# Optimization experiments

Measured on AMD Instinct MI355X. Metric: run time of the kernel, lower is better.

## Reference

```python
import jax, jax.numpy as jnp
import numpy as np

L = 1024   # latent_size
K = 8
R = L // K # 128 reduced dim
T = 32     # caption length
B = 64     # batch (images and captions)
DIN = 300  # word embedding dim
REG = 36   # image regions
R3 = 3 * R
H3 = 3 * L

def _p(key, shape, scale=0.05):
    return scale * jax.random.normal(key, shape, dtype=jnp.float32)

def setup_inputs():
    ks = jax.random.split(jax.random.key(0), 40)
    return {
        'img_embed': jax.random.normal(ks[0], (B, REG, L), jnp.float32),
        'cap_embed': jax.random.normal(ks[1], (B, T, DIN), jnp.float32),
        'lens': jax.random.randint(ks[2], (B,), 1, T + 1),
        'W_reduce_img': _p(ks[3], (R, L)), 'b_reduce_img': _p(ks[4], (R,)),
        'W_reduce_txt': _p(ks[5], (R, DIN)), 'b_reduce_txt': _p(ks[6], (R,)),
        'gru_Wih_f': _p(ks[7], (H3, DIN)), 'gru_Whh_f': _p(ks[8], (H3, L)),
        'gru_bih_f': _p(ks[9], (H3,)), 'gru_bhh_f': _p(ks[10], (H3,)),
        'gru_Wih_b': _p(ks[11], (H3, DIN)), 'gru_Whh_b': _p(ks[12], (H3, L)),
        'gru_bih_b': _p(ks[13], (H3,)), 'gru_bhh_b': _p(ks[14], (H3,)),
        'sa_Wq': _p(ks[15], (R, L)), 'sa_bq': _p(ks[16], (R,)),
        'sa_Wk': _p(ks[17], (R, L)), 'sa_bk': _p(ks[18], (R,)),
        'sa_Wv': _p(ks[19], (L, L)), 'sa_bv': _p(ks[20], (L,)),
        'sa_gamma': jnp.float32(0.5),
        'gen_Wih': _p(ks[21], (R3 * R, R)), 'gen_bih': _p(ks[22], (R3 * R,)),
        'gen_Whh': _p(ks[23], (R3 * R, R)), 'gen_bhh': _p(ks[24], (R3 * R,)),
        'gen_Wbih': _p(ks[25], (R3, R)), 'gen_bbih': _p(ks[26], (R3,)),
        'gen_Wbhh': _p(ks[27], (R3, R)), 'gen_bbhh': _p(ks[28], (R3,)),
        'W_txt_fc': _p(ks[29], (L, R + L)), 'b_txt_fc': _p(ks[30], (L,)),
    }

def l2norm(x, axis=-1, eps=1e-8):
    return x / (jnp.linalg.norm(x, axis=axis, keepdims=True) + eps)

def gru_dir(x, Wih, Whh, bih, bhh, reverse=False):
    # torch GRU math, gate order [r, z, n]; x: (B, T, D) -> (B, T, H)
    H = Whh.shape[1]
    gi = jnp.einsum('btd,hd->tbh', x, Wih) + bih  # precompute input gates (T, B, 3H)
    h0 = jnp.zeros((x.shape[0], H), x.dtype)
    def step(h, gi_t):
        gh = h @ Whh.T + bhh
        r = jax.nn.sigmoid(gi_t[:, :H] + gh[:, :H])
        z = jax.nn.sigmoid(gi_t[:, H:2 * H] + gh[:, H:2 * H])
        n = jnp.tanh(gi_t[:, 2 * H:] + r * gh[:, 2 * H:])
        hn = (1.0 - z) * n + z * h
        return hn, hn
    _, hs = jax.lax.scan(step, h0, gi, reverse=reverse)
    return jnp.swapaxes(hs, 0, 1)

def _forward(img_embed, cap_embed, lens, W_reduce_img, b_reduce_img, W_reduce_txt, b_reduce_txt,
             gru_Wih_f, gru_Whh_f, gru_bih_f, gru_bhh_f, gru_Wih_b, gru_Whh_b, gru_bih_b, gru_bhh_b,
             sa_Wq, sa_bq, sa_Wk, sa_bk, sa_Wv, sa_bv, sa_gamma,
             gen_Wih, gen_bih, gen_Whh, gen_bhh, gen_Wbih, gen_bbih, gen_Wbhh, gen_bbhh,
             W_txt_fc, b_txt_fc):
    # 1. bidirectional GRU over captions, average the two directions
    hf = gru_dir(cap_embed, gru_Wih_f, gru_Whh_f, gru_bih_f, gru_bhh_f, False)
    hb = gru_dir(cap_embed, gru_Wih_b, gru_Whh_b, gru_bih_b, gru_bhh_b, True)
    txt = (hf + hb) / 2.0                                   # (B, T, L)
    # 2. SAGAN-style 1D self-attention on (B, L, T)
    x = jnp.swapaxes(txt, 1, 2)                             # (B, L, T)
    q = jnp.einsum('bct,oc->bto', x, sa_Wq) + sa_bq          # (B, T, R)
    kk = jnp.einsum('bct,oc->bot', x, sa_Wk) + sa_bk[:, None]  # (B, R, T)
    attn = jax.nn.softmax(jnp.einsum('bto,bos->bts', q, kk), axis=-1)  # (B, T, T)
    v = jnp.einsum('bct,oc->bot', x, sa_Wv) + sa_bv[:, None]  # (B, L, T)
    x = sa_gamma * jnp.einsum('bcs,bts->bct', v, attn) + x
    # 3. length-masked mean pooling
    txt = jnp.swapaxes(x, 1, 2)                             # (B, T, L)
    mask = (jnp.arange(T)[None, :] < lens[:, None]).astype(txt.dtype)
    txt_embed = (txt * mask[:, :, None]).sum(1) / lens[:, None].astype(txt.dtype)  # (B, L)
    # 4. conv1d(k=1) reductions == linear over channel dim
    img = jnp.swapaxes(img_embed, 1, 2)                     # (B, L, REG)
    img_embed_global = img.mean(-1)                         # (B, L)
    cap_reduced = jnp.einsum('btd,od->btd2'.replace('d2','o'), cap_embed, W_reduce_txt) + b_reduce_txt  # (B, T, R)
    img_reduced = jnp.einsum('bcr,oc->bor', img, W_reduce_img) + b_reduce_img[:, None]  # (B, R, REG)
    img_global_vec = img_reduced.mean(-1)                   # (B, R)
    # 5. per-image generated-weight GRU over all captions (vmap replaces B-loop)
    def per_image(base, img_glob):
        Wih = (gen_Wih @ base + gen_bih).reshape(R3, R)
        Whh = (gen_Whh @ base + gen_bhh).reshape(R3, R)
        bih = gen_Wbih @ base + gen_bbih
        bhh = gen_Wbhh @ base + gen_bbhh
        gi = jnp.einsum('btd,hd->tbh', cap_reduced, Wih) + bih  # (T, B, 3R)
        h0 = jnp.zeros((cap_reduced.shape[0], R), cap_reduced.dtype)
        def step(h, gi_t):
            gh = h @ Whh.T + bhh
            r = jax.nn.sigmoid(gi_t[:, :R] + gh[:, :R])
            z = jax.nn.sigmoid(gi_t[:, R:2 * R] + gh[:, R:2 * R])
            n = jnp.tanh(gi_t[:, 2 * R:] + r * gh[:, 2 * R:])
            hn = (1.0 - z) * n + z * h
            return hn, hn
        _, hs = jax.lax.scan(step, h0, gi)                  # (T, B, R)
        txt_vec = hs.max(0)                                 # max over time -> (B, R)
        txt_vec = jnp.concatenate([txt_embed, txt_vec], axis=1) @ W_txt_fc.T + b_txt_fc
        txt_vec = l2norm(txt_vec)                           # (B, L)
        iv = l2norm(img_glob)                               # (L,)
        return txt_vec @ iv                                 # (B,) cosine sims for this image
    sims = jax.vmap(per_image)(img_global_vec, img_embed_global)  # (B_img, B_cap)
    return sims

def reference(img_embed, cap_embed, lens, W_reduce_img, b_reduce_img, W_reduce_txt, b_reduce_txt,
              gru_Wih_f, gru_Whh_f, gru_bih_f, gru_bhh_f, gru_Wih_b, gru_Whh_b, gru_bih_b, gru_bhh_b,
              sa_Wq, sa_bq, sa_Wk, sa_bk, sa_Wv, sa_bv, sa_gamma,
              gen_Wih, gen_bih, gen_Whh, gen_bhh, gen_Wbih, gen_bbih, gen_Wbhh, gen_bbhh,
              W_txt_fc, b_txt_fc):
    return _forward(img_embed, cap_embed, lens, W_reduce_img, b_reduce_img, W_reduce_txt, b_reduce_txt,
                    gru_Wih_f, gru_Whh_f, gru_bih_f, gru_bhh_f, gru_Wih_b, gru_Whh_b, gru_bih_b, gru_bhh_b,
                    sa_Wq, sa_bq, sa_Wk, sa_bk, sa_Wv, sa_bv, sa_gamma,
                    gen_Wih, gen_bih, gen_Whh, gen_bhh, gen_Wbih, gen_bbih, gen_Wbhh, gen_bbhh,
                    W_txt_fc, b_txt_fc)
```

## Files before the change

### kernel.cpp

```cpp
#include <hip/hip_runtime.h>
#include <math.h>

#define Lsz   1024
#define Tsz   32
#define Bsz   64
#define DIN   300
#define REG   36
#define Rsz   128
#define R3sz  384
#define H3sz  3072
#define GENROWS 49152
#define NC    2048
#define KPAD  304

typedef __attribute__((ext_vector_type(8))) short bf16x8;
typedef __attribute__((ext_vector_type(4))) float f32x4;

__device__ __forceinline__ float sigf(float x) { return 1.f / (1.f + __expf(-x)); }

__device__ __forceinline__ ushort f2bf(float x) {
    unsigned u = __float_as_uint(x);
    unsigned r = (u + 0x7fffu + ((u >> 16) & 1u)) >> 16;
    return (ushort)r;
}
__device__ __forceinline__ float bf2f(ushort h) {
    return __uint_as_float((unsigned)h << 16);
}


__device__ __forceinline__ size_t hfrag_off(int k, int b) {
    return (((size_t)(k >> 5) * 4 + (b >> 4)) * 64 +
            ((((k >> 3) & 3) << 4) | (b & 15))) * 8 + (k & 7);
}

__device__ __forceinline__ void pack8(const float* v, ushort* dsth, ushort* dstl) {
    unsigned hw[4], lw[4];
#pragma unroll
    for (int e2 = 0; e2 < 4; e2++) {
        ushort h0 = f2bf(v[2 * e2]);
        ushort h1 = f2bf(v[2 * e2 + 1]);
        ushort l0 = f2bf(v[2 * e2] - bf2f(h0));
        ushort l1 = f2bf(v[2 * e2 + 1] - bf2f(h1));
        hw[e2] = (unsigned)h0 | ((unsigned)h1 << 16);
        lw[e2] = (unsigned)l0 | ((unsigned)l1 << 16);
    }
    *(uint4*)dsth = make_uint4(hw[0], hw[1], hw[2], hw[3]);
    *(uint4*)dstl = make_uint4(lw[0], lw[1], lw[2], lw[3]);
}

__global__ __launch_bounds__(256) void transp_kernel(
    const float* __restrict__ in, float* __restrict__ out,
    int R, int Cin, int Cpad, int lda, int woff)
{
    __shared__ float s[64][65];
    int c0 = blockIdx.x * 64, r0 = blockIdx.y * 64;
    int tid = threadIdx.x;
#pragma unroll
    for (int l = 0; l < 16; l++) {
        int e = l * 256 + tid;
        int rr = e >> 6, cc = e & 63;
        int r = r0 + rr, c = c0 + cc;
        s[rr][cc] = (r < R && c < Cin) ? in[(size_t)r * lda + woff + c] : 0.f;
    }
    __syncthreads();
#pragma unroll
    for (int l = 0; l < 16; l++) {
        int e = l * 256 + tid;
        int cc = e >> 6, rr = e & 63;
        int c = c0 + cc, r = r0 + rr;
        if (c < Cpad && r < R) out[(size_t)c * R + r] = s[rr][cc];
    }
}

__global__ __launch_bounds__(256) void captr_kernel(
    const float* __restrict__ cap_embed, float* __restrict__ capTr)
{
    __shared__ float s[64][65];
    int t = blockIdx.x, kc = blockIdx.y;
    int tid = threadIdx.x;
#pragma unroll
    for (int l = 0; l < 16; l++) {
        int e = l * 256 + tid;
        int b = e >> 6, kk = e & 63;
        int k = kc * 64 + kk;
// ... 298 lines not shown
    for (int c = tid; c < Lsz; c += 256) {
        float s = 0.f;
        for (int r = 0; r < REG; r++) s += img_embed[((size_t)i * REG + r) * Lsz + c];
        row[c] = s * (1.f / (float)REG);
    }
    __syncthreads();
    float ss = 0.f;
    for (int c = tid; c < Lsz; c += 256) { float x = row[c]; ss = fmaf(x, x, ss); }
#pragma unroll
    for (int off = 32; off; off >>= 1) ss += __shfl_down(ss, off, 64);
    int lane = tid & 63, w = tid >> 6;
    if (lane == 0) ps[w] = ss;
    __syncthreads();
    float inv = 1.f / (sqrtf(ps[0] + ps[1] + ps[2] + ps[3]) + 1e-8f);
    for (int c = tid; c < Lsz; c += 256)
        iv[(size_t)i * Lsz + c] = row[c] * inv;
    for (int o = w * 32; o < w * 32 + 32; o++) {
        float a = 0.f;
        const float* wr = W_reduce_img + (size_t)o * Lsz + lane * 16;
        const float* rr = row + lane * 16;
#pragma unroll
        for (int u = 0; u < 16; u++) a = fmaf(wr[u], rr[u], a);
#pragma unroll
        for (int off = 32; off; off >>= 1) a += __shfl_down(a, off, 64);
        if (lane == 0) base[(size_t)i * Rsz + o] = a + b_reduce_img[o];
    }
}

__global__ __launch_bounds__(256) void packwhh_kernel(
    const float* __restrict__ Wf, const float* __restrict__ Wb,
    float* __restrict__ WFh_, float* __restrict__ WFl_)
{
    int tid = threadIdx.x;
    int l = tid & 63, wid = tid >> 6;
    int k0 = blockIdx.x * 4 + wid;
    int mstrip = blockIdx.y;
    int dir = blockIdx.z;
    const float* W = dir ? Wb : Wf;
    int row = mstrip * 16 + (l & 15);
    int col = k0 * 32 + (l >> 4) * 8;
    float v[8];
    *(float4*)&v[0] = *(const float4*)&W[(size_t)row * Lsz + col];
    *(float4*)&v[4] = *(const float4*)&W[(size_t)row * Lsz + col + 4];
    size_t off = ((size_t)(dir * 192 + mstrip) * 32 + k0) * 512 + l * 8;
    pack8(v, (ushort*)WFh_ + off, (ushort*)WFl_ + off);
}

__global__ __launch_bounds__(256) void packgenw_kernel(
    const float* __restrict__ WihAllT, const float* __restrict__ WhhAllT,
    float* __restrict__ GFh_, float* __restrict__ GFl_)
{
    int tid = threadIdx.x;
    int l = tid & 63, kt = tid >> 6;
    int mstrip = blockIdx.x;
    int mat = blockIdx.y;
    int i = blockIdx.z;
    const float* W = (mat ? WhhAllT : WihAllT) + (size_t)i * GENROWS;
    int row = mstrip * 16 + (l & 15);
    int kb = kt * 32 + (l >> 4) * 8;
    float v[8];
#pragma unroll
    for (int e = 0; e < 8; e++)
        v[e] = W[(size_t)(kb + e) * R3sz + row];
    size_t off = (((size_t)(i * 2 + mat) * 24 + mstrip) * 4 + kt) * 512 + l * 8;
    pack8(v, (ushort*)GFh_ + off, (ushort*)GFl_ + off);
}

__global__ __launch_bounds__(256) void packcap_kernel(
    const float* __restrict__ capT2, float* __restrict__ CFh_, float* __restrict__ CFl_)
{
    int tid = threadIdx.x;
    int l = tid & 63, kt = tid >> 6;
    int ctp = blockIdx.x;
    int col = ctp * 16 + (l & 15);
    int kb = kt * 32 + (l >> 4) * 8;
    float v[8];
#pragma unroll
    for (int e = 0; e < 8; e++)
        v[e] = capT2[(size_t)(kb + e) * NC + col];
    size_t off = ((size_t)kt * 128 + ctp) * 512 + l * 8;
    pack8(v, (ushort*)CFh_ + off, (ushort*)CFl_ + off);
}

__global__ __launch_bounds__(256) void step_fused(
    const float* __restrict__ WhhF_h, const float* __restrict__ WhhF_l,
    const float* __restrict__ WgenF_h, const float* __restrict__ WgenF_l,
    const float* __restrict__ capF_h, const float* __restrict__ capF_l,
    float* __restrict__ capHF_h, float* __restrict__ capHF_l,
    float* __restrict__ genHF_h, float* __restrict__ genHF_l,
    const float* __restrict__ giT2_f, const float* __restrict__ giT2_b,
    float* __restrict__ hfT, float* __restrict__ hbT,
    const float* __restrict__ bhh_f, const float* __restrict__ bhh_b,
    const float* __restrict__ bihAll, const float* __restrict__ bhhAll,
    const float* __restrict__ hprevT, float* __restrict__ hcurT,
    float* __restrict__ hmaxT, int step)
{
    __shared__ float red[48 * 256];
    int tid = threadIdx.x, l = tid & 63, wid = tid >> 6;
    int bid = blockIdx.x;
    int ping = (step & 1) ^ 1;
    int pong = step & 1;

    if (bid < 128) {
        int dir = bid >> 6, js = bid & 63;
        f32x4 acc[3][4];
#pragma unroll
        for (int g = 0; g < 3; g++)
#pragma unroll
            for (int ct = 0; ct < 4; ct++) acc[g][ct] = (f32x4){0.f, 0.f, 0.f, 0.f};

        if (step > 0) {
            const ushort* Wh = (const ushort*)WhhF_h + (size_t)dir * (192 * 32 * 512);
            const ushort* Wl = (const ushort*)WhhF_l + (size_t)dir * (192 * 32 * 512);
            const ushort* Hh = (const ushort*)capHF_h + (size_t)(dir * 2 + ping) * 65536;
            const ushort* Hl = (const ushort*)capHF_l + (size_t)(dir * 2 + ping) * 65536;
            for (int k8 = 0; k8 < 8; k8++) {
                int k0 = wid * 8 + k8;
                bf16x8 Bh[4], Bl[4], Ah[3], Al[3];
#pragma unroll
                for (int ct = 0; ct < 4; ct++) {
                    size_t fo = ((size_t)k0 * 4 + ct) * 512 + l * 8;
                    Bh[ct] = *(const bf16x8*)(Hh + fo);
                    Bl[ct] = *(const bf16x8*)(Hl + fo);
                }
#pragma unroll
                for (int g = 0; g < 3; g++) {
                    size_t fo = ((size_t)(g * 64 + js) * 32 + k0) * 512 + l * 8;
                    Ah[g] = *(const bf16x8*)(Wh + fo);
                    Al[g] = *(const bf16x8*)(Wl + fo);
                }
#pragma unroll
                for (int g = 0; g < 3; g++)
#pragma unroll
                    for (int ct = 0; ct < 4; ct++)
                        acc[g][ct] = __builtin_amdgcn_mfma_f32_16x16x32_bf16(
                            Ah[g], Bh[ct], acc[g][ct], 0, 0, 0);
#pragma unroll
                for (int g = 0; g < 3; g++)
#pragma unroll
                    for (int ct = 0; ct < 4; ct++)
                        acc[g][ct] = __builtin_amdgcn_mfma_f32_16x16x32_bf16(
                            Ah[g], Bl[ct], acc[g][ct], 0, 0, 0);
#pragma unroll
                for (int g = 0; g < 3; g++)
#pragma unroll
                    for (int ct = 0; ct < 4; ct++)
                        acc[g][ct] = __builtin_amdgcn_mfma_f32_16x16x32_bf16(
                            Al[g], Bh[ct], acc[g][ct], 0, 0, 0);
            }
        }
#pragma unroll
        for (int g = 0; g < 3; g++)
#pragma unroll
            for (int ct = 0; ct < 4; ct++)
                *(f32x4*)&red[((wid * 3 + g) * 4 + ct) * 256 + l * 4] = acc[g][ct];
        __syncthreads();

        const float* giT = dir ? giT2_b : giT2_f;
        float* hT        = dir ? hbT   : hfT;
        const float* bhh = dir ? bhh_b : bhh_f;
        int t  = dir ? (Tsz - 1 - step) : step;
        int tp = dir ? (t + 1) : (t - 1);
        ushort* Ch = (ushort*)capHF_h + (size_t)(dir * 2 + pong) * 65536;
        ushort* Cl = (ushort*)capHF_l + (size_t)(dir * 2 + pong) * 65536;
#pragma unroll
        for (int u = 0; u < 4; u++) {
            int e = u * 256 + tid;
            int jj = e >> 6, b = e & 63;
            int j = js * 16 + jj;
            float gh[3] = {0.f, 0.f, 0.f};
            if (step > 0) {
                int lane_ = ((jj >> 2) << 4) | (b & 15);
                int reg = jj & 3, ct = b >> 4;
#pragma unroll
                for (int w = 0; w < 4; w++)
#pragma unroll
                    for (int g = 0; g < 3; g++)
                        gh[g] += red[((w * 3 + g) * 4 + ct) * 256 + lane_ * 4 + reg];
            }
            size_t gc = (size_t)t * 64 + b;
            float gr = giT[(size_t)j * NC + gc];
            float gz = giT[((size_t)Lsz + j) * NC + gc];
            float gn = giT[((size_t)2 * Lsz + j) * NC + gc];
            float hp = (step > 0) ? hT[((size_t)tp * Lsz + j) * Bsz + b] : 0.f;
            float r = sigf(gr + gh[0] + bhh[j]);
            float z = sigf(gz + gh[1] + bhh[Lsz + j]);
            float n = tanhf(gn + r * (gh[2] + bhh[2 * Lsz + j]));
            float h = (1.f - z) * n + z * hp;
            hT[((size_t)t * Lsz + j) * Bsz + b] = h;
            size_t fo = hfrag_off(j, b);
            ushort hb = f2bf(h);
            Ch[fo] = hb;
            Cl[fo] = f2bf(h - bf2f(hb));
        }
    } else {
        int g2 = bid - 128;
        int i = g2 >> 2;
        int p = g2 & 3;
        int mat = wid & 1;
        int sl = wid >> 1;
        int strip = p * 2 + sl;
        f32x4 acc[3][4];
#pragma unroll
        for (int g = 0; g < 3; g++)
#pragma unroll
            for (int ct = 0; ct < 4; ct++) acc[g][ct] = (f32x4){0.f, 0.f, 0.f, 0.f};

        if (mat == 0 || step > 0) {
            const ushort* Ahp = (const ushort*)WgenF_h + (size_t)(i * 2 + mat) * 96 * 512;
            const ushort* Alp = (const ushort*)WgenF_l + (size_t)(i * 2 + mat) * 96 * 512;
            const ushort* Bhp;
            const ushort* Blp;
            if (mat == 0) {
                Bhp = (const ushort*)capF_h;
                Blp = (const ushort*)capF_l;
            } else {
                Bhp = (const ushort*)genHF_h + (size_t)(ping * 64 + i) * 8192;
                Blp = (const ushort*)genHF_l + (size_t)(ping * 64 + i) * 8192;
            }
            for (int kt = 0; kt < 4; kt++) {
                bf16x8 Bh[4], Bl[4], Ah[3], Al[3];
#pragma unroll
                for (int ct = 0; ct < 4; ct++) {
                    size_t fo = (mat == 0)
                        ? ((size_t)kt * 128 + step * 4 + ct) * 512 + l * 8
                        : ((size_t)kt * 4 + ct) * 512 + l * 8;
                    Bh[ct] = *(const bf16x8*)(Bhp + fo);
                    Bl[ct] = *(const bf16x8*)(Blp + fo);
                }
#pragma unroll
                for (int g = 0; g < 3; g++) {
                    size_t fo = ((size_t)(g * 8 + strip) * 4 + kt) * 512 + l * 8;
                    Ah[g] = *(const bf16x8*)(Ahp + fo);
                    Al[g] = *(const bf16x8*)(Alp + fo);
                }
#pragma unroll
                for (int g = 0; g < 3; g++)
#pragma unroll
                    for (int ct = 0; ct < 4; ct++)
                        acc[g][ct] = __builtin_amdgcn_mfma_f32_16x16x32_bf16(
                            Ah[g], Bh[ct], acc[g][ct], 0, 0, 0);
#pragma unroll
                for (int g = 0; g < 3; g++)
#pragma unroll
                    for (int ct = 0; ct < 4; ct++)
                        acc[g][ct] = __builtin_amdgcn_mfma_f32_16x16x32_bf16(
                            Ah[g], Bl[ct], acc[g][ct], 0, 0, 0);
#pragma unroll
                for (int g = 0; g < 3; g++)
#pragma unroll
                    for (int ct = 0; ct < 4; ct++)
                        acc[g][ct] = __builtin_amdgcn_mfma_f32_16x16x32_bf16(
                            Al[g], Bh[ct], acc[g][ct], 0, 0, 0);
            }
        }
#pragma unroll
        for (int g = 0; g < 3; g++)
#pragma unroll
            for (int ct = 0; ct < 4; ct++)
                *(f32x4*)&red[(((sl * 2 + mat) * 3 + g) * 4 + ct) * 256 + l * 4] = acc[g][ct];
        __syncthreads();

        const float* bih = bihAll + (size_t)i * R3sz;
        const float* bhh = bhhAll + (size_t)i * R3sz;
        ushort* Gh = (ushort*)genHF_h + (size_t)(pong * 64 + i) * 8192;
        ushort* Gl = (ushort*)genHF_l + (size_t)(pong * 64 + i) * 8192;
#pragma unroll
        for (int u = 0; u < 8; u++) {
            int e = u * 256 + tid;
            int sl2 = e >> 10;
            int jj = (e >> 6) & 15;
            int b = e & 63;
            int j = (p * 2 + sl2) * 16 + jj;
            int lane_ = ((jj >> 2) << 4) | (b & 15);
            int reg = jj & 3, ct = b >> 4;
            float sih[3], shh[3];
#pragma unroll
            for (int g = 0; g < 3; g++) {
                sih[g] = red[(((sl2 * 2 + 0) * 3 + g) * 4 + ct) * 256 + lane_ * 4 + reg];
                shh[g] = (step > 0)
                    ? red[(((sl2 * 2 + 1) * 3 + g) * 4 + ct) * 256 + lane_ * 4 + reg]
                    : 0.f;
            }
            float r = sigf(sih[0] + bih[j] + shh[0] + bhh[j]);
            float z = sigf(sih[1] + bih[Rsz + j] + shh[1] + bhh[Rsz + j]);
            float n = tanhf(sih[2] + bih[2 * Rsz + j] + r * (shh[2] + bhh[2 * Rsz + j]));
            float hp = (step > 0) ? hprevT[((size_t)i * Rsz + j) * Bsz + b] : 0.f;
            float h = (1.f - z) * n + z * hp;
            size_t idx = ((size_t)i * Rsz + j) * Bsz + b;
            hcurT[idx] = h;
            hmaxT[idx] = (step == 0) ? h : fmaxf(hmaxT[idx], h);
            size_t fo = hfrag_off(j, b);
            ushort hb = f2bf(h);
            Gh[fo] = hb;
            Gl[fo] = f2bf(h - bf2f(hb));
        }
    }
}

__global__ __launch_bounds__(256) void txt_combine(
    const float* __restrict__ hfT, const float* __restrict__ hbT,
    float* __restrict__ txt, float* __restrict__ txtT)
{
    __shared__ float s[64][65];
    int t = blockIdx.x;
    int c0 = blockIdx.y * 64;
    int tid = threadIdx.x;
#pragma unroll
    for (int l = 0; l < 16; l++) {
        int e = l * 256 + tid;
        int cc = e >> 6, b = e & 63;
        size_t idx = ((size_t)t * Lsz + c0 + cc) * Bsz + b;
        s[cc][b] = 0.5f * (hfT[idx] + hbT[idx]);
    }
    __syncthreads();
#pragma unroll
    for (int l = 0; l < 16; l++) {
        int e = l * 256 + tid;
        int b = e >> 6, cc = e & 63;
        txt[((size_t)b * Tsz + t) * Lsz + c0 + cc] = s[cc][b];
    }
#pragma unroll
    for (int l = 0; l < 16; l++) {
        int e = l * 256 + tid;
        int cc = e >> 6, b = e & 63;
        txtT[(size_t)(c0 + cc) * NC + t * 64 + b] = s[cc][b];
    }
}

__global__ __launch_bounds__(256) void attn_kernel(
    const float* __restrict__ q, const float* __restrict__ kmat,
    const float* __restrict__ vP, const float* __restrict__ sa_bv,
    const float* __restrict__ txt,
    const float* __restrict__ gamma_p, float* __restrict__ xattn)
{
    __shared__ float qs[32][129];
    __shared__ float ks[32][129];
    __shared__ float Sc[32][33];
    __shared__ float vs[128][33];
    int b = blockIdx.x;
    int c0 = blockIdx.y * 128;
    int tid = threadIdx.x;
    for (int e = tid; e < Tsz * Rsz; e += 256) {
        qs[e >> 7][e & 127] = q[(size_t)b * Tsz * Rsz + e];
        ks[e >> 7][e & 127] = kmat[(size_t)b * Tsz * Rsz + e];
    }
    for (int e = tid; e < 128 * 32; e += 256) {
        int cc = e >> 5, ss = e & 31;
        size_t base = (size_t)(c0 + cc) * NC + ss * 64 + b;
        float v = sa_bv[c0 + cc];
#pragma unroll
        for (int z = 0; z < 2; z++)
            v += vP[(size_t)z * Lsz * NC + base];
        vs[cc][ss] = v;
    }
    __syncthreads();
    for (int e = tid; e < Tsz * Tsz; e += 256) {
        int t = e >> 5, ss = e & 31;
        float acc = 0.f;
#pragma unroll 4
        for (int o = 0; o < Rsz; o++) acc = fmaf(qs[t][o], ks[ss][o], acc);
        Sc[t][ss] = acc;
    }
    __syncthreads();
    if (tid < 32) {
        int t = tid;
        float mx = -1e30f;
#pragma unroll
        for (int ss = 0; ss < 32; ss++) mx = fmaxf(mx, Sc[t][ss]);
        float sum = 0.f;
        float ex[32];
#pragma unroll
        for (int ss = 0; ss < 32; ss++) { ex[ss] = __expf(Sc[t][ss] - mx); sum += ex[ss]; }
        float inv = 1.f / sum;
#pragma unroll
        for (int ss = 0; ss < 32; ss++) Sc[t][ss] = ex[ss] * inv;
    }
    __syncthreads();
// ... 70 lines not shown
        int c = cs * 256 + w * 64 + u;
        float f = fcT[(size_t)c * 4096 + i * 64 + b] + base_fcT[(size_t)c * Bsz + b] + bfc[c];
        s1 = fmaf(f, f, s1);
        s2 = fmaf(f, iv[(size_t)i * Lsz + c], s2);
    }
    int m = i * 64 + b;
    atomicAdd(&accA[m], s1);
    atomicAdd(&accB[m], s2);
}

__global__ __launch_bounds__(256) void sims_final(
    const float* __restrict__ accA, const float* __restrict__ accB,
    float* __restrict__ out)
{
    int m = blockIdx.x * 256 + threadIdx.x;
    out[m] = accB[m] / (sqrtf(accA[m]) + 1e-8f);
}

extern "C" void kernel_launch(void* const* d_in, const int* in_sizes, int n_in,
                              void* d_out, int out_size, void* d_ws, size_t ws_size,
                              hipStream_t stream)
{
    const float* img_embed    = (const float*)d_in[0];
    const float* cap_embed    = (const float*)d_in[1];
    const int*   lens         = (const int*)d_in[2];
    const float* W_reduce_img = (const float*)d_in[3];
    const float* b_reduce_img = (const float*)d_in[4];
    const float* W_reduce_txt = (const float*)d_in[5];
    const float* b_reduce_txt = (const float*)d_in[6];
    const float* gru_Wih_f    = (const float*)d_in[7];
    const float* gru_Whh_f    = (const float*)d_in[8];
    const float* gru_bih_f    = (const float*)d_in[9];
    const float* gru_bhh_f    = (const float*)d_in[10];
    const float* gru_Wih_b    = (const float*)d_in[11];
    const float* gru_Whh_b    = (const float*)d_in[12];
    const float* gru_bih_b    = (const float*)d_in[13];
    const float* gru_bhh_b    = (const float*)d_in[14];
    const float* sa_Wq        = (const float*)d_in[15];
    const float* sa_bq        = (const float*)d_in[16];
    const float* sa_Wk        = (const float*)d_in[17];
    const float* sa_bk        = (const float*)d_in[18];
    const float* sa_Wv        = (const float*)d_in[19];
    const float* sa_bv        = (const float*)d_in[20];
    const float* sa_gamma     = (const float*)d_in[21];
    const float* gen_Wih      = (const float*)d_in[22];
    const float* gen_bih      = (const float*)d_in[23];
    const float* gen_Whh      = (const float*)d_in[24];
    const float* gen_bhh      = (const float*)d_in[25];
    const float* gen_Wbih     = (const float*)d_in[26];
    const float* gen_bbih     = (const float*)d_in[27];
    const float* gen_Wbhh     = (const float*)d_in[28];
    const float* gen_bbhh     = (const float*)d_in[29];
    const float* W_txt_fc     = (const float*)d_in[30];
    const float* b_txt_fc     = (const float*)d_in[31];

    float* ws = (float*)d_ws;
    size_t off = 0;
    auto alloc = [&](size_t n) { float* p = ws + off; off += n; return p; };
    float* giT2_f   = alloc((size_t)H3sz * NC);
    float* giT2_b   = alloc((size_t)H3sz * NC);
    float* hfT      = alloc((size_t)Tsz * Lsz * Bsz);
    float* hbT      = alloc((size_t)Tsz * Lsz * Bsz);
    float* capTr    = alloc((size_t)KPAD * NC);
    float* capT2    = alloc((size_t)Rsz * NC);
    float* txt      = alloc((size_t)Bsz * Tsz * Lsz);
    float* txtT     = alloc((size_t)Lsz * NC);
    float* qbuf     = alloc((size_t)Bsz * Tsz * Rsz);
    float* kbuf     = alloc((size_t)Bsz * Tsz * Rsz);
    float* pool     = alloc((size_t)12582912);
    float* WhhFh  = pool;
    float* WhhFl  = pool + 3145728;
    float* WgenFh = pool + 6291456;
    float* WgenFl = pool + 9437184;
    float* qP  = pool;
    float* kP  = pool + 2097152;
    float* vP  = pool + 4194304;
    float* fcT = pool + 8388608;
    float* xattn    = alloc((size_t)Bsz * Tsz * Lsz);
    float* txt_emb  = alloc((size_t)Bsz * Lsz);
    float* base     = alloc((size_t)Bsz * Rsz);
    float* iv       = alloc((size_t)Bsz * Lsz);
    float* WihAllT  = alloc((size_t)Bsz * GENROWS);
    float* WhhAllT  = alloc((size_t)Bsz * GENROWS);
    float* WihT_f   = alloc((size_t)KPAD * H3sz);
    float* WihT_b   = alloc((size_t)KPAD * H3sz);
    float* WrtT     = alloc((size_t)KPAD * Rsz);
    float* WvT      = alloc((size_t)Lsz * Lsz);
    float* WqT      = alloc((size_t)Lsz * Rsz);
    float* WkT      = alloc((size_t)Lsz * Rsz);
    float* WfcT     = alloc((size_t)Rsz * Lsz);
    float* bihAll   = alloc((size_t)Bsz * R3sz);
    float* bhhAll   = alloc((size_t)Bsz * R3sz);
    float* hA       = alloc((size_t)Bsz * Rsz * Bsz);
    float* hB       = alloc((size_t)Bsz * Rsz * Bsz);
    float* hmaxT    = alloc((size_t)Bsz * Rsz * Bsz);
    float* hstdT    = alloc((size_t)Rsz * Bsz * Bsz);
    float* base_fcT = alloc((size_t)Lsz * Bsz);
    float* accA     = alloc(4096);
    float* accB     = alloc(4096);
    float* capFh    = alloc(131072);
    float* capFl    = alloc(131072);
    float* capHFh   = alloc(131072);
    float* capHFl   = alloc(131072);
    float* genHFh   = alloc(524288);
    float* genHFl   = alloc(524288);

    hipMemsetAsync(accA, 0, 2 * 4096 * sizeof(float), stream);

    transp_kernel<<<dim3(5, 48), 256, 0, stream>>>(gru_Wih_f, WihT_f, H3sz, DIN, KPAD, DIN, 0);
    transp_kernel<<<dim3(5, 48), 256, 0, stream>>>(gru_Wih_b, WihT_b, H3sz, DIN, KPAD, DIN, 0);
    transp_kernel<<<dim3(5, 2), 256, 0, stream>>>(W_reduce_txt, WrtT, Rsz, DIN, KPAD, DIN, 0);
    transp_kernel<<<dim3(16, 16), 256, 0, stream>>>(sa_Wv, WvT, Lsz, Lsz, Lsz, Lsz, 0);
    transp_kernel<<<dim3(16, 2), 256, 0, stream>>>(sa_Wq, WqT, Rsz, Lsz, Lsz, Lsz, 0);
    transp_kernel<<<dim3(16, 2), 256, 0, stream>>>(sa_Wk, WkT, Rsz, Lsz, Lsz, Lsz, 0);
    transp_kernel<<<dim3(2, 16), 256, 0, stream>>>(W_txt_fc, WfcT, Lsz, Rsz, Rsz, Rsz + Lsz, Lsz);
    captr_kernel<<<dim3(32, 5), 256, 0, stream>>>(cap_embed, capTr);

    img_kernel<<<64, 256, 0, stream>>>(img_embed, W_reduce_img, b_reduce_img, base, iv);
    genw_gemm<<<dim3(3, 129, 2), 256, 0, stream>>>(gen_Wih, gen_bih, gen_Whh, gen_bhh,
        gen_Wbih, gen_bbih, gen_Wbhh, gen_bbhh, base, WihAllT, WhhAllT, bihAll, bhhAll);
    packwhh_kernel<<<dim3(8, 192, 2), 256, 0, stream>>>(gru_Whh_f, gru_Whh_b, WhhFh, WhhFl);
    packgenw_kernel<<<dim3(24, 2, 64), 256, 0, stream>>>(WihAllT, WhhAllT, WgenFh, WgenFl);

    gemm_tt<<<dim3(16, 24, 2), 256, 0, stream>>>(WihT_f, WihT_b, capTr,
        gru_bih_f, gru_bih_b, giT2_f, giT2_b, H3sz);
    gemm_tt<<<dim3(16, 1, 1), 256, 0, stream>>>(WrtT, WrtT, capTr,
        b_reduce_txt, b_reduce_txt, capT2, capT2, Rsz);
    packcap_kernel<<<128, 256, 0, stream>>>(capT2, capFh, capFl);

    for (int s = 0; s < Tsz; s++) {
        const float* hp = (s & 1) ? hA : hB;
        float* hc = (s & 1) ? hB : hA;
        if (s == 0) hp = hA;
        step_fused<<<384, 256, 0, stream>>>(WhhFh, WhhFl, WgenFh, WgenFl,
            capFh, capFl, capHFh, capHFl, genHFh, genHFl,
            giT2_f, giT2_b, hfT, hbT, gru_bhh_f, gru_bhh_b,
            bihAll, bhhAll, hp, hc, hmaxT, s);
    }
    hstdT_kernel<<<64, 256, 0, stream>>>(hmaxT, hstdT);

    txt_combine<<<dim3(32, 16), 256, 0, stream>>>(hfT, hbT, txt, txtT);
    gemm_qk<<<dim3(16, 2, 8), 256, 0, stream>>>(WqT, WkT, txtT, qP, kP);
    gemm_ttp<<<dim3(16, 8, 2), 256, 0, stream>>>(WvT, txtT, vP, Lsz, NC, 512);
    qkc_kernel<<<dim3(32, 2), 256, 0, stream>>>(qP, kP, sa_bq, sa_bk, qbuf, kbuf);
    attn_kernel<<<dim3(64, 8), 256, 0, stream>>>(qbuf, kbuf, vP, sa_bv, txt,
        sa_gamma, xattn);

    pool_kernel<<<dim3(64, 4), 256, 0, stream>>>(xattn, lens, txt_emb);
    basefc_kernel<<<256, 256, 0, stream>>>(txt_emb, W_txt_fc, base_fcT);

    gemm_ttp<<<dim3(32, 8, 1), 256, 0, stream>>>(WfcT, hstdT, fcT, Lsz, 4096, Rsz);
    sims_part<<<dim3(64, 4), 256, 0, stream>>>(fcT, base_fcT, b_txt_fc, iv, accA, accB);
    sims_final<<<16, 256, 0, stream>>>(accA, accB, (float*)d_out);
}
```

Before: 1.363 ms.

## Make GRU recurrence one persistent cooperative kernel and move input-gate GEMM to MFMA

```diff
diff --git a/kernel.cpp b/kernel.cpp
--- a/kernel.cpp
+++ b/kernel.cpp
@@ -1,5 +1,8 @@
 #include <hip/hip_runtime.h>
+#include <hip/hip_cooperative_groups.h>
 #include <math.h>
+
+namespace cg = cooperative_groups;
 
 #define Lsz   1024
 #define Tsz   32
@@ -464,218 +467,337 @@
     pack8(v, (ushort*)CFh_ + off, (ushort*)CFl_ + off);
 }
 
-__global__ __launch_bounds__(256) void step_fused(
+__global__ __launch_bounds__(256) void packwih_kernel(
+    const float* __restrict__ Wf, const float* __restrict__ Wb,
+    float* __restrict__ Fh, float* __restrict__ Fl)
+{
+    int tid = threadIdx.x, l = tid & 63, wid = tid >> 6;
+    int kt = blockIdx.x * 4 + wid;
+    int m = blockIdx.y, dir = blockIdx.z;
+    if (kt >= 10) return;
+    const float* W = dir ? Wb : Wf;
+    int row = m * 16 + (l & 15);
+    int kb = kt * 32 + (l >> 4) * 8;
+    float v[8];
+#pragma unroll
+    for (int e = 0; e < 8; e++) {
+        int k = kb + e;
+        v[e] = (k < DIN) ? W[(size_t)row * DIN + k] : 0.f;
+    }
+    size_t off = (((size_t)dir * 192 + m) * 10 + kt) * 512 + l * 8;
+    pack8(v, (ushort*)Fh + off, (ushort*)Fl + off);
+}
+
+__global__ __launch_bounds__(256) void packcapb_kernel(
+    const float* __restrict__ cap_embed, float* __restrict__ Fh, float* __restrict__ Fl)
+{
+    int tid = threadIdx.x, l = tid & 63, wid = tid >> 6;
+    int ct = blockIdx.x;
+    int kt = blockIdx.y * 4 + wid;
+    if (kt >= 10) return;
+    int c = ct * 16 + (l & 15), t = c >> 6, b = c & 63;
+    int kb = kt * 32 + (l >> 4) * 8;
+    float v[8];
+#pragma unroll
+    for (int e = 0; e < 8; e++) {
+        int k = kb + e;
+        v[e] = (k < DIN) ? cap_embed[((size_t)b * Tsz + t) * DIN + k] : 0.f;
+    }
+    size_t off = ((size_t)kt * 128 + ct) * 512 + l * 8;
+    pack8(v, (ushort*)Fh + off, (ushort*)Fl + off);
+}
+
+__global__ __launch_bounds__(256) void gi_mfma(
+    const float* __restrict__ WihF_h, const float* __restrict__ WihF_l,
+    const float* __restrict__ capBF_h, const float* __restrict__ capBF_l,
+    const float* __restrict__ bih_f, const float* __restrict__ bih_b,
+    float* __restrict__ giT2_f, float* __restrict__ giT2_b)
+{
+    __shared__ __align__(16) ushort BsH[8][512];
+    __shared__ __align__(16) ushort BsL[8][512];
+    int tid = threadIdx.x, l = tid & 63, wid = tid >> 6;
+    int ctg = blockIdx.x, mg = blockIdx.y, dir = blockIdx.z;
+    int ct0 = ctg * 8;
+    int m0 = mg * 8 + wid * 2;
+    const ushort* AH = (const ushort*)WihF_h + (size_t)dir * (192 * 10 * 512);
+    const ushort* AL = (const ushort*)WihF_l + (size_t)dir * (192 * 10 * 512);
+    const ushort* BH = (const ushort*)capBF_h;
+    const ushort* BL = (const ushort*)capBF_l;
+    const float* bias = dir ? bih_b : bih_f;
+    float* C = dir ? giT2_b : giT2_f;
+
+    f32x4 acc[2][8];
+#pragma unroll
+    for (int m = 0; m < 2; m++)
+#pragma unroll
+        for (int ct = 0; ct < 8; ct++) acc[m][ct] = (f32x4){0.f, 0.f, 0.f, 0.f};
+
+    for (int kt = 0; kt < 10; kt++) {
+        __syncthreads();
+#pragma unroll
+        for (int u = 0; u < 2; u++) {
+            int e = u * 256 + tid;
+            int ct = e >> 6, p8 = (e & 63) * 8;
+            *(uint4*)&BsH[ct][p8] = *(const uint4*)&BH[((size_t)kt * 128 + ct0 + ct) * 512 + p8];
+            *(uint4*)&BsL[ct][p8] = *(const uint4*)&BL[((size_t)kt * 128 + ct0 + ct) * 512 + p8];
+        }
+        __syncthreads();
+        bf16x8 Ah[2], Al[2];
+#pragma unroll
+        for (int m = 0; m < 2; m++) {
+            size_t ao = ((size_t)(m0 + m) * 10 + kt) * 512 + l * 8;
+            Ah[m] = *(const bf16x8*)(AH + ao);
+            Al[m] = *(const bf16x8*)(AL + ao);
+        }
+#pragma unroll
+        for (int ct = 0; ct < 8; ct++) {
+            bf16x8 Bh = *(const bf16x8*)&BsH[ct][l * 8];
+            bf16x8 Bl = *(const bf16x8*)&BsL[ct][l * 8];
+#pragma unroll
+            for (int m = 0; m < 2; m++) {
+                acc[m][ct] = __builtin_amdgcn_mfma_f32_16x16x32_bf16(Ah[m], Bh, acc[m][ct], 0, 0, 0);
+                acc[m][ct] = __builtin_amdgcn_mfma_f32_16x16x32_bf16(Ah[m], Bl, acc[m][ct], 0, 0, 0);
+                acc[m][ct] = __builtin_amdgcn_mfma_f32_16x16x32_bf16(Al[m], Bh, acc[m][ct], 0, 0, 0);
+            }
+        }
+    }
+    int row4 = (l >> 4) * 4, col = l & 15;
+#pragma unroll
+    for (int m = 0; m < 2; m++) {
+        int nb_ = (m0 + m) * 16 + row4;
+#pragma unroll
+        for (int r = 0; r < 4; r++) {
+            float bv = bias[nb_ + r];
+#pragma unroll
+            for (int ct = 0; ct < 8; ct++)
+                C[(size_t)(nb_ + r) * NC + (size_t)(ct0 + ct) * 16 + col] = acc[m][ct][r] + bv;
+        }
+    }
+}
+
+template <bool COOP>
+__global__ __launch_bounds__(256) void rec_kernel(
     const float* __restrict__ WhhF_h, const float* __restrict__ WhhF_l,
     const float* __restrict__ WgenF_h, const float* __restrict__ WgenF_l,
     const float* __restrict__ capF_h, const float* __restrict__ capF_l,
-    float* __restrict__ capHF_h, float* __restrict__ capHF_l,
-    float* __restrict__ genHF_h, float* __restrict__ genHF_l,
+    float* capHF_h, float* capHF_l,
+    float* genHF_h, float* genHF_l,
     const float* __restrict__ giT2_f, const float* __restrict__ giT2_b,
-    float* __restrict__ hfT, float* __restrict__ hbT,
+    float* hfT, float* hbT,
     const float* __restrict__ bhh_f, const float* __restrict__ bhh_b,
     const float* __restrict__ bihAll, const float* __restrict__ bhhAll,
-    const float* __restrict__ hprevT, float* __restrict__ hcurT,
-    float* __restrict__ hmaxT, int step)
+    float* hA, float* hB, float* hmaxT,
+    int s0, int s1)
 {
     __shared__ float red[48 * 256];
     int tid = threadIdx.x, l = tid & 63, wid = tid >> 6;
     int bid = blockIdx.x;
-    int ping = (step & 1) ^ 1;
-    int pong = step & 1;
-
-    if (bid < 128) {
-        int dir = bid >> 6, js = bid & 63;
-        f32x4 acc[3][4];
-#pragma unroll
-        for (int g = 0; g < 3; g++)
-#pragma unroll
-            for (int ct = 0; ct < 4; ct++) acc[g][ct] = (f32x4){0.f, 0.f, 0.f, 0.f};
-
-        if (step > 0) {
-            const ushort* Wh = (const ushort*)WhhF_h + (size_t)dir * (192 * 32 * 512);
-            const ushort* Wl = (const ushort*)WhhF_l + (size_t)dir * (192 * 32 * 512);
-            const ushort* Hh = (const ushort*)capHF_h + (size_t)(dir * 2 + ping) * 65536;
-            const ushort* Hl = (const ushort*)capHF_l + (size_t)(dir * 2 + ping) * 65536;
-            for (int k8 = 0; k8 < 8; k8++) {
-                int k0 = wid * 8 + k8;
-                bf16x8 Bh[4], Bl[4], Ah[3], Al[3];
-#pragma unroll
-                for (int ct = 0; ct < 4; ct++) {
-                    size_t fo = ((size_t)k0 * 4 + ct) * 512 + l * 8;
-                    Bh[ct] = *(const bf16x8*)(Hh + fo);
-                    Bl[ct] = *(const bf16x8*)(Hl + fo);
+
+    for (int s = s0; s < s1; ++s) {
+        int ping = (s & 1) ^ 1;
+        int pong = s & 1;
+
+        if (bid < 128) {
+            int dir = bid >> 6, js = bid & 63;
+            f32x4 acc[3][4];
+#pragma unroll
+            for (int g = 0; g < 3; g++)
+#pragma unroll
+                for (int ct = 0; ct < 4; ct++) acc[g][ct] = (f32x4){0.f, 0.f, 0.f, 0.f};
+
+            if (s > 0) {
+                const ushort* Wh = (const ushort*)WhhF_h + (size_t)dir * (192 * 32 * 512);
+                const ushort* Wl = (const ushort*)WhhF_l + (size_t)dir * (192 * 32 * 512);
+                const ushort* Hh = (const ushort*)capHF_h + (size_t)(dir * 2 + ping) * 65536;
+                const ushort* Hl = (const ushort*)capHF_l + (size_t)(dir * 2 + ping) * 65536;
+                for (int k8 = 0; k8 < 8; k8++) {
+                    int k0 = wid * 8 + k8;
+                    bf16x8 Bh[4], Bl[4], Ah[3], Al[3];
+#pragma unroll
+                    for (int ct = 0; ct < 4; ct++) {
+                        size_t fo = ((size_t)k0 * 4 + ct) * 512 + l * 8;
+                        Bh[ct] = *(const bf16x8*)(Hh + fo);
+                        Bl[ct] = *(const bf16x8*)(Hl + fo);
+                    }
+#pragma unroll
+                    for (int g = 0; g < 3; g++) {
+                        size_t fo = ((size_t)(g * 64 + js) * 32 + k0) * 512 + l * 8;
+                        Ah[g] = *(const bf16x8*)(Wh + fo);
+                        Al[g] = *(const bf16x8*)(Wl + fo);
+                    }
+#pragma unroll
+                    for (int g = 0; g < 3; g++)
+#pragma unroll
+                        for (int ct = 0; ct < 4; ct++)
+                            acc[g][ct] = __builtin_amdgcn_mfma_f32_16x16x32_bf16(
+                                Ah[g], Bh[ct], acc[g][ct], 0, 0, 0);
+#pragma unroll
+                    for (int g = 0; g < 3; g++)
+#pragma unroll
+                        for (int ct = 0; ct < 4; ct++)
+                            acc[g][ct] = __builtin_amdgcn_mfma_f32_16x16x32_bf16(
+                                Ah[g], Bl[ct], acc[g][ct], 0, 0, 0);
+#pragma unroll
+                    for (int g = 0; g < 3; g++)
+#pragma unroll
+                        for (int ct = 0; ct < 4; ct++)
+                            acc[g][ct] = __builtin_amdgcn_mfma_f32_16x16x32_bf16(
+                                Al[g], Bh[ct], acc[g][ct], 0, 0, 0);
                 }
-#pragma unroll
-                for (int g = 0; g < 3; g++) {
-                    size_t fo = ((size_t)(g * 64 + js) * 32 + k0) * 512 + l * 8;
-                    Ah[g] = *(const bf16x8*)(Wh + fo);
-                    Al[g] = *(const bf16x8*)(Wl + fo);
+            }
+#pragma unroll
+            for (int g = 0; g < 3; g++)
+#pragma unroll
+                for (int ct = 0; ct < 4; ct++)
+                    *(f32x4*)&red[((wid * 3 + g) * 4 + ct) * 256 + l * 4] = acc[g][ct];
+            __syncthreads();
+
+            const float* giT = dir ? giT2_b : giT2_f;
+            float* hT        = dir ? hbT   : hfT;
+            const float* bhh = dir ? bhh_b : bhh_f;
+            int t  = dir ? (Tsz - 1 - s) : s;
+            int tp = dir ? (t + 1) : (t - 1);
+            ushort* Ch = (ushort*)capHF_h + (size_t)(dir * 2 + pong) * 65536;
+            ushort* Cl = (ushort*)capHF_l + (size_t)(dir * 2 + pong) * 65536;
+#pragma unroll
+            for (int u = 0; u < 4; u++) {
+                int e = u * 256 + tid;
+                int jj = e >> 6, b = e & 63;
+                int j = js * 16 + jj;
+                float gh[3] = {0.f, 0.f, 0.f};
+                if (s > 0) {
+                    int lane_ = ((jj >> 2) << 4) | (b & 15);
+                    int reg = jj & 3, ct = b >> 4;
+#pragma unroll
+                    for (int w = 0; w < 4; w++)
+#pragma unroll
+                        for (int g = 0; g < 3; g++)
+                            gh[g] += red[((w * 3 + g) * 4 + ct) * 256 + lane_ * 4 + reg];
                 }
-#pragma unroll
-                for (int g = 0; g < 3; g++)
-#pragma unroll
-                    for (int ct = 0; ct < 4; ct++)
-                        acc[g][ct] = __builtin_amdgcn_mfma_f32_16x16x32_bf16(
-                            Ah[g], Bh[ct], acc[g][ct], 0, 0, 0);
-#pragma unroll
-                for (int g = 0; g < 3; g++)
-#pragma unroll
-                    for (int ct = 0; ct < 4; ct++)
-                        acc[g][ct] = __builtin_amdgcn_mfma_f32_16x16x32_bf16(
-                            Ah[g], Bl[ct], acc[g][ct], 0, 0, 0);
-#pragma unroll
-                for (int g = 0; g < 3; g++)
-#pragma unroll
-                    for (int ct = 0; ct < 4; ct++)
-                        acc[g][ct] = __builtin_amdgcn_mfma_f32_16x16x32_bf16(
-                            Al[g], Bh[ct], acc[g][ct], 0, 0, 0);
+                size_t gc = (size_t)t * 64 + b;
+                float gr = giT[(size_t)j * NC + gc];
+                float gz = giT[((size_t)Lsz + j) * NC + gc];
+                float gn = giT[((size_t)2 * Lsz + j) * NC + gc];
+                float hp = (s > 0) ? hT[((size_t)tp * Lsz + j) * Bsz + b] : 0.f;
+                float r = sigf(gr + gh[0] + bhh[j]);
+                float z = sigf(gz + gh[1] + bhh[Lsz + j]);
+                float n = tanhf(gn + r * (gh[2] + bhh[2 * Lsz + j]));
+                float h = (1.f - z) * n + z * hp;
+                hT[((size_t)t * Lsz + j) * Bsz + b] = h;
+                size_t fo = hfrag_off(j, b);
+                ushort hb = f2bf(h);
+                Ch[fo] = hb;
+                Cl[fo] = f2bf(h - bf2f(hb));
             }
-        }
-#pragma unroll
-        for (int g = 0; g < 3; g++)
-#pragma unroll
-            for (int ct = 0; ct < 4; ct++)
-                *(f32x4*)&red[((wid * 3 + g) * 4 + ct) * 256 + l * 4] = acc[g][ct];
-        __syncthreads();
-
-        const float* giT = dir ? giT2_b : giT2_f;
-        float* hT        = dir ? hbT   : hfT;
-        const float* bhh = dir ? bhh_b : bhh_f;
-        int t  = dir ? (Tsz - 1 - step) : step;
-        int tp = dir ? (t + 1) : (t - 1);
-        ushort* Ch = (ushort*)capHF_h + (size_t)(dir * 2 + pong) * 65536;
-        ushort* Cl = (ushort*)capHF_l + (size_t)(dir * 2 + pong) * 65536;
-#pragma unroll
-        for (int u = 0; u < 4; u++) {
-            int e = u * 256 + tid;
-            int jj = e >> 6, b = e & 63;
-            int j = js * 16 + jj;
-            float gh[3] = {0.f, 0.f, 0.f};
-            if (step > 0) {
+        } else {
+            int g2 = bid - 128;
+            int i = g2 >> 2;
+            int p = g2 & 3;
+            int mat = wid & 1;
+            int sl = wid >> 1;
+            int strip = p * 2 + sl;
+            float* hcurT = (s & 1) ? hB : hA;
+            const float* hprevT = (s & 1) ? hA : hB;
+            f32x4 acc[3][4];
+#pragma unroll
+            for (int g = 0; g < 3; g++)
+#pragma unroll
+                for (int ct = 0; ct < 4; ct++) acc[g][ct] = (f32x4){0.f, 0.f, 0.f, 0.f};
+
+            if (mat == 0 || s > 0) {
+                const ushort* Ahp = (const ushort*)WgenF_h + (size_t)(i * 2 + mat) * 96 * 512;
+                const ushort* Alp = (const ushort*)WgenF_l + (size_t)(i * 2 + mat) * 96 * 512;
+                const ushort* Bhp;
+                const ushort* Blp;
+                if (mat == 0) {
+                    Bhp = (const ushort*)capF_h;
+                    Blp = (const ushort*)capF_l;
+                } else {
+                    Bhp = (const ushort*)genHF_h + (size_t)(ping * 64 + i) * 8192;
+                    Blp = (const ushort*)genHF_l + (size_t)(ping * 64 + i) * 8192;
+                }
+                for (int kt = 0; kt < 4; kt++) {
+                    bf16x8 Bh[4], Bl[4], Ah[3], Al[3];
+#pragma unroll
+                    for (int ct = 0; ct < 4; ct++) {
+                        size_t fo = (mat == 0)
+                            ? ((size_t)kt * 128 + s * 4 + ct) * 512 + l * 8
+                            : ((size_t)kt * 4 + ct) * 512 + l * 8;
+                        Bh[ct] = *(const bf16x8*)(Bhp + fo);
+                        Bl[ct] = *(const bf16x8*)(Blp + fo);
+                    }
+#pragma unroll
+                    for (int g = 0; g < 3; g++) {
+                        size_t fo = ((size_t)(g * 8 + strip) * 4 + kt) * 512 + l * 8;
+                        Ah[g] = *(const bf16x8*)(Ahp + fo);
+                        Al[g] = *(const bf16x8*)(Alp + fo);
+                    }
+#pragma unroll
+                    for (int g = 0; g < 3; g++)
+#pragma unroll
+                        for (int ct = 0; ct < 4; ct++)
+                            acc[g][ct] = __builtin_amdgcn_mfma_f32_16x16x32_bf16(
+                                Ah[g], Bh[ct], acc[g][ct], 0, 0, 0);
+#pragma unroll
+                    for (int g = 0; g < 3; g++)
+#pragma unroll
+                        for (int ct = 0; ct < 4; ct++)
+                            acc[g][ct] = __builtin_amdgcn_mfma_f32_16x16x32_bf16(
+                                Ah[g], Bl[ct], acc[g][ct], 0, 0, 0);
+#pragma unroll
+                    for (int g = 0; g < 3; g++)
+#pragma unroll
+                        for (int ct = 0; ct < 4; ct++)
+                            acc[g][ct] = __builtin_amdgcn_mfma_f32_16x16x32_bf16(
+                                Al[g], Bh[ct], acc[g][ct], 0, 0, 0);
+                }
+            }
+#pragma unroll
+            for (int g = 0; g < 3; g++)
+#pragma unroll
+                for (int ct = 0; ct < 4; ct++)
+                    *(f32x4*)&red[(((sl * 2 + mat) * 3 + g) * 4 + ct) * 256 + l * 4] = acc[g][ct];
+            __syncthreads();
+
+            const float* bih = bihAll + (size_t)i * R3sz;
+            const float* bhh = bhhAll + (size_t)i * R3sz;
+            ushort* Gh = (ushort*)genHF_h + (size_t)(pong * 64 + i) * 8192;
+            ushort* Gl = (ushort*)genHF_l + (size_t)(pong * 64 + i) * 8192;
+#pragma unroll
+            for (int u = 0; u < 8; u++) {
+                int e = u * 256 + tid;
+                int sl2 = e >> 10;
+                int jj = (e >> 6) & 15;
+                int b = e & 63;
+                int j = (p * 2 + sl2) * 16 + jj;
                 int lane_ = ((jj >> 2) << 4) | (b & 15);
                 int reg = jj & 3, ct = b >> 4;
-#pragma unroll
-                for (int w = 0; w < 4; w++)
-#pragma unroll
-                    for (int g = 0; g < 3; g++)
-                        gh[g] += red[((w * 3 + g) * 4 + ct) * 256 + lane_ * 4 + reg];
+                float sih[3], shh[3];
+#pragma unroll
+                for (int g = 0; g < 3; g++) {
+                    sih[g] = red[(((sl2 * 2 + 0) * 3 + g) * 4 + ct) * 256 + lane_ * 4 + reg];
+                    shh[g] = (s > 0)
+                        ? red[(((sl2 * 2 + 1) * 3 + g) * 4 + ct) * 256 + lane_ * 4 + reg]
+                        : 0.f;
+                }
+                float r = sigf(sih[0] + bih[j] + shh[0] + bhh[j]);
+                float z = sigf(sih[1] + bih[Rsz + j] + shh[1] + bhh[Rsz + j]);
+                float n = tanhf(sih[2] + bih[2 * Rsz + j] + r * (shh[2] + bhh[2 * Rsz + j]));
+                float hp = (s > 0) ? hprevT[((size_t)i * Rsz + j) * Bsz + b] : 0.f;
+                float h = (1.f - z) * n + z * hp;
+                size_t idx = ((size_t)i * Rsz + j) * Bsz + b;
+                hcurT[idx] = h;
+                hmaxT[idx] = (s == 0) ? h : fmaxf(hmaxT[idx], h);
+                size_t fo = hfrag_off(j, b);
+                ushort hb = f2bf(h);
+                Gh[fo] = hb;
+                Gl[fo] = f2bf(h - bf2f(hb));
             }
-            size_t gc = (size_t)t * 64 + b;
-            float gr = giT[(size_t)j * NC + gc];
-            float gz = giT[((size_t)Lsz + j) * NC + gc];
-            float gn = giT[((size_t)2 * Lsz + j) * NC + gc];
-            float hp = (step > 0) ? hT[((size_t)tp * Lsz + j) * Bsz + b] : 0.f;
-            float r = sigf(gr + gh[0] + bhh[j]);
-            float z = sigf(gz + gh[1] + bhh[Lsz + j]);
-            float n = tanhf(gn + r * (gh[2] + bhh[2 * Lsz + j]));
-            float h = (1.f - z) * n + z * hp;
-            hT[((size_t)t * Lsz + j) * Bsz + b] = h;
-            size_t fo = hfrag_off(j, b);
-            ushort hb = f2bf(h);
-            Ch[fo] = hb;
-            Cl[fo] = f2bf(h - bf2f(hb));
-        }
-    } else {
-        int g2 = bid - 128;
-        int i = g2 >> 2;
-        int p = g2 & 3;
-        int mat = wid & 1;
-        int sl = wid >> 1;
-        int strip = p * 2 + sl;
-        f32x4 acc[3][4];
-#pragma unroll
-        for (int g = 0; g < 3; g++)
-#pragma unroll
-            for (int ct = 0; ct < 4; ct++) acc[g][ct] = (f32x4){0.f, 0.f, 0.f, 0.f};
-
-        if (mat == 0 || step > 0) {
-            const ushort* Ahp = (const ushort*)WgenF_h + (size_t)(i * 2 + mat) * 96 * 512;
-            const ushort* Alp = (const ushort*)WgenF_l + (size_t)(i * 2 + mat) * 96 * 512;
-            const ushort* Bhp;
-            const ushort* Blp;
-            if (mat == 0) {
-                Bhp = (const ushort*)capF_h;
-                Blp = (const ushort*)capF_l;
-            } else {
-                Bhp = (const ushort*)genHF_h + (size_t)(ping * 64 + i) * 8192;
-                Blp = (const ushort*)genHF_l + (size_t)(ping * 64 + i) * 8192;
-            }
-            for (int kt = 0; kt < 4; kt++) {
-                bf16x8 Bh[4], Bl[4], Ah[3], Al[3];
-#pragma unroll
-                for (int ct = 0; ct < 4; ct++) {
-                    size_t fo = (mat == 0)
-                        ? ((size_t)kt * 128 + step * 4 + ct) * 512 + l * 8
-                        : ((size_t)kt * 4 + ct) * 512 + l * 8;
-                    Bh[ct] = *(const bf16x8*)(Bhp + fo);
-                    Bl[ct] = *(const bf16x8*)(Blp + fo);
-                }
-#pragma unroll
-                for (int g = 0; g < 3; g++) {
-                    size_t fo = ((size_t)(g * 8 + strip) * 4 + kt) * 512 + l * 8;
-                    Ah[g] = *(const bf16x8*)(Ahp + fo);
-                    Al[g] = *(const bf16x8*)(Alp + fo);
-                }
-#pragma unroll
-                for (int g = 0; g < 3; g++)
-#pragma unroll
-                    for (int ct = 0; ct < 4; ct++)
-                        acc[g][ct] = __builtin_amdgcn_mfma_f32_16x16x32_bf16(
-                            Ah[g], Bh[ct], acc[g][ct], 0, 0, 0);
-#pragma unroll
-                for (int g = 0; g < 3; g++)
-#pragma unroll
-                    for (int ct = 0; ct < 4; ct++)
-                        acc[g][ct] = __builtin_amdgcn_mfma_f32_16x16x32_bf16(
-                            Ah[g], Bl[ct], acc[g][ct], 0, 0, 0);
-#pragma unroll
-                for (int g = 0; g < 3; g++)
-#pragma unroll
-                    for (int ct = 0; ct < 4; ct++)
-                        acc[g][ct] = __builtin_amdgcn_mfma_f32_16x16x32_bf16(
-                            Al[g], Bh[ct], acc[g][ct], 0, 0, 0);
-            }
-        }
-#pragma unroll
-        for (int g = 0; g < 3; g++)
-#pragma unroll
-            for (int ct = 0; ct < 4; ct++)
-                *(f32x4*)&red[(((sl * 2 + mat) * 3 + g) * 4 + ct) * 256 + l * 4] = acc[g][ct];
-        __syncthreads();
-
-        const float* bih = bihAll + (size_t)i * R3sz;
-        const float* bhh = bhhAll + (size_t)i * R3sz;
-        ushort* Gh = (ushort*)genHF_h + (size_t)(pong * 64 + i) * 8192;
-        ushort* Gl = (ushort*)genHF_l + (size_t)(pong * 64 + i) * 8192;
-#pragma unroll
-        for (int u = 0; u < 8; u++) {
-            int e = u * 256 + tid;
-            int sl2 = e >> 10;
-            int jj = (e >> 6) & 15;
-            int b = e & 63;
-            int j = (p * 2 + sl2) * 16 + jj;
-            int lane_ = ((jj >> 2) << 4) | (b & 15);
-            int reg = jj & 3, ct = b >> 4;
-            float sih[3], shh[3];
-#pragma unroll
-            for (int g = 0; g < 3; g++) {
-                sih[g] = red[(((sl2 * 2 + 0) * 3 + g) * 4 + ct) * 256 + lane_ * 4 + reg];
-                shh[g] = (step > 0)
-                    ? red[(((sl2 * 2 + 1) * 3 + g) * 4 + ct) * 256 + lane_ * 4 + reg]
-                    : 0.f;
-            }
-            float r = sigf(sih[0] + bih[j] + shh[0] + bhh[j]);
-            float z = sigf(sih[1] + bih[Rsz + j] + shh[1] + bhh[Rsz + j]);
-            float n = tanhf(sih[2] + bih[2 * Rsz + j] + r * (shh[2] + bhh[2 * Rsz + j]));
-            float hp = (step > 0) ? hprevT[((size_t)i * Rsz + j) * Bsz + b] : 0.f;
-            float h = (1.f - z) * n + z * hp;
-            size_t idx = ((size_t)i * Rsz + j) * Bsz + b;
-            hcurT[idx] = h;
-            hmaxT[idx] = (step == 0) ? h : fmaxf(hmaxT[idx], h);
-            size_t fo = hfrag_off(j, b);
-            ushort hb = f2bf(h);
-            Gh[fo] = hb;
-            Gl[fo] = f2bf(h - bf2f(hb));
+        }
+
+        if constexpr (COOP) {
+            __threadfence();
+            cg::this_grid().sync();
         }
     }
 }
@@ -912,8 +1034,10 @@
     float* iv       = alloc((size_t)Bsz * Lsz);
     float* WihAllT  = alloc((size_t)Bsz * GENROWS);
     float* WhhAllT  = alloc((size_t)Bsz * GENROWS);
-    float* WihT_f   = alloc((size_t)KPAD * H3sz);
-    float* WihT_b   = alloc((size_t)KPAD * H3sz);
+    float* WihFh    = alloc((size_t)983040);
+    float* WihFl    = alloc((size_t)983040);
+    float* capBFh   = alloc((size_t)327680);
+    float* capBFl   = alloc((size_t)327680);
     float* WrtT     = alloc((size_t)KPAD * Rsz);
     float* WvT      = alloc((size_t)Lsz * Lsz);
     float* WqT      = alloc((size_t)Lsz * Rsz);
@@ -937,14 +1061,14 @@
 
     hipMemsetAsync(accA, 0, 2 * 4096 * sizeof(float), stream);
 
-    transp_kernel<<<dim3(5, 48), 256, 0, stream>>>(gru_Wih_f, WihT_f, H3sz, DIN, KPAD, DIN, 0);
-    transp_kernel<<<dim3(5, 48), 256, 0, stream>>>(gru_Wih_b, WihT_b, H3sz, DIN, KPAD, DIN, 0);
     transp_kernel<<<dim3(5, 2), 256, 0, stream>>>(W_reduce_txt, WrtT, Rsz, DIN, KPAD, DIN, 0);
     transp_kernel<<<dim3(16, 16), 256, 0, stream>>>(sa_Wv, WvT, Lsz, Lsz, Lsz, Lsz, 0);
     transp_kernel<<<dim3(16, 2), 256, 0, stream>>>(sa_Wq, WqT, Rsz, Lsz, Lsz, Lsz, 0);
     transp_kernel<<<dim3(16, 2), 256, 0, stream>>>(sa_Wk, WkT, Rsz, Lsz, Lsz, Lsz, 0);
     transp_kernel<<<dim3(2, 16), 256, 0, stream>>>(W_txt_fc, WfcT, Lsz, Rsz, Rsz, Rsz + Lsz, Lsz);
     captr_kernel<<<dim3(32, 5), 256, 0, stream>>>(cap_embed, capTr);
+    packwih_kernel<<<dim3(3, 192, 2), 256, 0, stream>>>(gru_Wih_f, gru_Wih_b, WihFh, WihFl);
+    packcapb_kernel<<<dim3(128, 3), 256, 0, stream>>>(cap_embed, capBFh, capBFl);
 
     img_kernel<<<64, 256, 0, stream>>>(img_embed, W_reduce_img, b_reduce_img, base, iv);
     genw_gemm<<<dim3(3, 129, 2), 256, 0, stream>>>(gen_Wih, gen_bih, gen_Whh, gen_bhh,
@@ -952,20 +1076,34 @@
     packwhh_kernel<<<dim3(8, 192, 2), 256, 0, stream>>>(gru_Whh_f, gru_Whh_b, WhhFh, WhhFl);
     packgenw_kernel<<<dim3(24, 2, 64), 256, 0, stream>>>(WihAllT, WhhAllT, WgenFh, WgenFl);
 
-    gemm_tt<<<dim3(16, 24, 2), 256, 0, stream>>>(WihT_f, WihT_b, capTr,
-        gru_bih_f, gru_bih_b, giT2_f, giT2_b, H3sz);
+    gi_mfma<<<dim3(16, 24, 2), 256, 0, stream>>>(WihFh, WihFl, capBFh, capBFl,
+        gru_bih_f, gru_bih_b, giT2_f, giT2_b);
     gemm_tt<<<dim3(16, 1, 1), 256, 0, stream>>>(WrtT, WrtT, capTr,
         b_reduce_txt, b_reduce_txt, capT2, capT2, Rsz);
     packcap_kernel<<<128, 256, 0, stream>>>(capT2, capFh, capFl);
 
-    for (int s = 0; s < Tsz; s++) {
-        const float* hp = (s & 1) ? hA : hB;
-        float* hc = (s & 1) ? hB : hA;
-        if (s == 0) hp = hA;
-        step_fused<<<384, 256, 0, stream>>>(WhhFh, WhhFl, WgenFh, WgenFl,
-            capFh, capFl, capHFh, capHFl, genHFh, genHFl,
-            giT2_f, giT2_b, hfT, hbT, gru_bhh_f, gru_bhh_b,
-            bihAll, bhhAll, hp, hc, hmaxT, s);
+    {
+        int s0 = 0, s1 = Tsz;
+        void* kargs[] = {
+            (void*)&WhhFh, (void*)&WhhFl, (void*)&WgenFh, (void*)&WgenFl,
+            (void*)&capFh, (void*)&capFl, (void*)&capHFh, (void*)&capHFl,
+            (void*)&genHFh, (void*)&genHFl, (void*)&giT2_f, (void*)&giT2_b,
+            (void*)&hfT, (void*)&hbT, (void*)&gru_bhh_f, (void*)&gru_bhh_b,
+            (void*)&bihAll, (void*)&bhhAll, (void*)&hA, (void*)&hB,
+            (void*)&hmaxT, (void*)&s0, (void*)&s1
+        };
+        int nb = 0;
+        hipOccupancyMaxActiveBlocksPerMultiprocessor(&nb, rec_kernel<true>, 256, 0);
+        if (nb >= 2) {
+            hipLaunchCooperativeKernel((void*)rec_kernel<true>, dim3(384), dim3(256),
+                                       kargs, 0, stream);
+        } else {
+            for (int s = 0; s < Tsz; s++)
+                rec_kernel<false><<<384, 256, 0, stream>>>(WhhFh, WhhFl, WgenFh, WgenFl,
+                    capFh, capFl, capHFh, capHFl, genHFh, genHFl, giT2_f, giT2_b,
+                    hfT, hbT, gru_bhh_f, gru_bhh_b, bihAll, bhhAll, hA, hB, hmaxT,
+                    s, s + 1);
+        }
     }
     hstdT_kernel<<<64, 256, 0, stream>>>(hmaxT, hstdT);
 
```

Measured after the change: 1.654 ms. 21.3% more time.
